# Kernel tuning notes

Hardware: AMD Instinct MI355X
Metric: run time of the kernel (lower is better)

Reference implementation:

```python
import jax, jax.numpy as jnp
import numpy as np
import math

B, D_MODEL, H, D_K, L = 24, 128, 8, 16, 512


def setup_inputs() -> dict:
    key = jax.random.key(0)
    ks = jax.random.split(key, 5)
    x = jax.random.normal(ks[0], (B, D_MODEL, L), dtype=jnp.float32)
    Wq = jax.random.normal(ks[1], (H, B, D_K, D_MODEL), dtype=jnp.float32)
    Wk = jax.random.normal(ks[2], (H, B, D_K, D_MODEL), dtype=jnp.float32)
    Wv = jax.random.normal(ks[3], (H, B, D_K, D_MODEL), dtype=jnp.float32)
    Wo = jax.random.normal(ks[4], (B, H * D_K, D_MODEL), dtype=jnp.float32)
    return {"x": x, "Wq": Wq, "Wk": Wk, "Wv": Wv, "Wo": Wo}


def reference(x, Wq, Wk, Wv, Wo):
    # Per-head, per-batch projections: [h,b,k,d] @ [b,d,l] -> [h,b,k,l]
    Q = jnp.einsum('hbkd,bdl->hbkl', Wq, x)
    K = jnp.einsum('hbkd,bdl->hbkl', Wk, x)
    V = jnp.einsum('hbkd,bdl->hbkl', Wv, x)
    # scores[h,b,l,m] = Q[:, :, :, l] . K[:, :, :, m]; torch softmax dim=1 of
    # the [B, L, L] score -> softmax over the QUERY axis l (axis=2 here).
    scores = jnp.einsum('hbkl,hbkm->hblm', Q, K) / math.sqrt(D_K)
    attn = jax.nn.softmax(scores, axis=2)
    # head_i = V @ attn : [h,b,v,l] @ [h,b,l,m] -> [h,b,v,m]
    heads = jnp.einsum('hbvl,hblm->hbvm', V, attn)
    # concat heads along channel dim: [b, h*v, L]
    head = heads.transpose(1, 0, 2, 3).reshape(B, H * D_K, L)
    # out = Wo @ head : [b, h*v, d_model] treated as [b,128,128] @ [b,128,L]
    out = jnp.einsum('bod,bdl->bol', Wo, head)
    return out
```

## Files before the change

kernel.cpp:

```cpp
#include <hip/hip_runtime.h>
#include <math.h>

#define NB 24
#define DM 128
#define NH 8
#define DK 16
#define LL 512
#define HB (NH * NB)

#define XTH_OFF 0
#define XTL_OFF 3145728
#define HT_OFF  6291456

typedef __attribute__((ext_vector_type(8))) short bf16x8;
typedef __attribute__((ext_vector_type(4))) float f32x4;
typedef __attribute__((ext_vector_type(4))) int   i32x4;

#define MFMA  __builtin_amdgcn_mfma_f32_16x16x32_bf16
#define EXP2  __builtin_amdgcn_exp2f
#define BPERM __builtin_amdgcn_ds_bpermute

static __device__ __forceinline__ unsigned bfr(float x) {
    return (__float_as_uint(x) + 0x8000u) & 0xffff0000u;
}

static __device__ __forceinline__ unsigned cvtpk(float a, float b) {
    unsigned r;
    asm("v_cvt_pk_bf16_f32 %0, %1, %2" : "=v"(r) : "v"(a), "v"(b));
    return r;
}

static __device__ __forceinline__ void wsplit(const float* __restrict__ p,
                                              bf16x8& aH, bf16x8& aL) {
    const float4 f0 = *(const float4*)p;
    const float4 f1 = *(const float4*)(p + 4);
    const float f[8] = {f0.x, f0.y, f0.z, f0.w, f1.x, f1.y, f1.z, f1.w};
    i32x4 h, l;
    #pragma unroll
    for (int q = 0; q < 4; ++q) {
        const unsigned h0 = bfr(f[2 * q]), h1 = bfr(f[2 * q + 1]);
        const unsigned e0 = bfr(f[2 * q]     - __uint_as_float(h0));
        const unsigned e1 = bfr(f[2 * q + 1] - __uint_as_float(h1));
        h[q] = (int)((h0 >> 16) | (h1 & 0xffff0000u));
        l[q] = (int)((e0 >> 16) | (e1 & 0xffff0000u));
    }
    aH = __builtin_bit_cast(bf16x8, h);
    aL = __builtin_bit_cast(bf16x8, l);
}

__global__ __launch_bounds__(256)
void prep(const float* __restrict__ x,
          unsigned short* __restrict__ xthi,
          unsigned short* __restrict__ xtlo)
{
    __shared__ float T[64][65];
    const int bid = blockIdx.x, tid = threadIdx.x;
    const int b = bid >> 3, lc = bid & 7;

    #pragma unroll
    for (int half = 0; half < 2; ++half) {
        const int d0 = half << 6;
        const float* __restrict__ xb =
            x + (size_t)b * 65536 + (size_t)d0 * LL + lc * 64;
        if (half) __syncthreads();
        #pragma unroll
        for (int i = 0; i < 16; ++i) {
            const int idx = i * 256 + tid;
            T[idx >> 6][idx & 63] = xb[(size_t)(idx >> 6) * LL + (idx & 63)];
        }
        __syncthreads();
        #pragma unroll
        for (int i = 0; i < 8; ++i) {
            const int idx = (i * 256 + tid) * 2;
            const int l = idx >> 6, dd = idx & 63;
            const float v0 = T[dd][l], v1 = T[dd + 1][l];
            const unsigned h0 = bfr(v0), h1 = bfr(v1);
            const unsigned e0 = bfr(v0 - __uint_as_float(h0));
            const unsigned e1 = bfr(v1 - __uint_as_float(h1));
            const size_t o = (size_t)b * 65536 +
                             (size_t)(lc * 64 + l) * DM + d0 + dd;
            *(unsigned*)(xthi + o) = (h0 >> 16) | (h1 & 0xffff0000u);
            *(unsigned*)(xtlo + o) = (e0 >> 16) | (e1 & 0xffff0000u);
        }
    }
}

static __device__ __forceinline__ void soft_pv(
    const f32x4& s0, const f32x4& s1, float tm, float& bar, float& sm,
    f32x4& O, const bf16x8& aV, int aLo, int aHi, bool up)
{
    const float nb = fmaxf(bar, tm + 32.f);
    const float f  = EXP2(bar - nb);
    bar = nb;
    const float e0 = EXP2(s0[0] - nb), e1 = EXP2(s0[1] - nb);
    const float e2 = EXP2(s0[2] - nb), e3 = EXP2(s0[3] - nb);
    const float e4 = EXP2(s1[0] - nb), e5 = EXP2(s1[1] - nb);
    const float e6 = EXP2(s1[2] - nb), e7 = EXP2(s1[3] - nb);
    const float sacc = ((e0 + e1) + (e2 + e3)) + ((e4 + e5) + (e6 + e7));
    sm = fmaf(sm, f, sacc);
    O *= f;
    const unsigned c0 = cvtpk(e0, e1), c1 = cvtpk(e2, e3);
    const unsigned c2 = cvtpk(e4, e5), c3 = cvtpk(e6, e7);
    const int p00 = BPERM(aLo, (int)c0), p02 = BPERM(aLo, (int)c2);
    const int p10 = BPERM(aLo, (int)c1), p12 = BPERM(aLo, (int)c3);
    const int p20 = BPERM(aHi, (int)c0), p22 = BPERM(aHi, (int)c2);
    const int p30 = BPERM(aHi, (int)c1), p32 = BPERM(aHi, (int)c3);
    i32x4 bi = { up ? p00 : p02, up ? p10 : p12,
                 up ? p20 : p22, up ? p30 : p32 };
    O = MFMA(aV, __builtin_bit_cast(bf16x8, bi), O, 0, 0, 0);
}

#define QK_STRIDE 40
#define V_STRIDE  520
#define KROWS     256

__global__ __launch_bounds__(512, 4)
void qkv_attn(const unsigned short* __restrict__ xthi,
              const unsigned short* __restrict__ xtlo,
              const float* __restrict__ Wq,
              const float* __restrict__ Wk,
              const float* __restrict__ Wv,
              unsigned short* __restrict__ ht)
{
    __shared__ unsigned short qs[LL * QK_STRIDE];
    __shared__ unsigned short ks[KROWS * QK_STRIDE];
    __shared__ unsigned short vs[DK * V_STRIDE];

    const int hb    = blockIdx.x >> 1;
    const int mhalf = blockIdx.x & 1;
    const int b     = hb % NB;
    const int wv    = threadIdx.x >> 6;
    const int lane  = threadIdx.x & 63;
    const int g     = lane >> 4;
    const int mR    = lane & 15;
    const int lQ    = wv * 64;
    const int kloc  = wv * 32;

    {
        const float* __restrict__ wqp = Wq + (size_t)hb * 2048 + mR * 128 + g * 8;
        const float* __restrict__ wkp = Wk + (size_t)hb * 2048 + mR * 128 + g * 8;
        const float* __restrict__ wvp = Wv + (size_t)hb * 2048 + mR * 128 + g * 8;
        const unsigned short* __restrict__ xh = xthi + (size_t)b * 65536 + g * 8;
        const unsigned short* __restrict__ xl = xtlo + (size_t)b * 65536 + g * 8;

        f32x4 CQ[4], CV[4], CK[2];
        #pragma unroll
        for (int t = 0; t < 4; ++t) {
            CQ[t] = (f32x4){0.f, 0.f, 0.f, 0.f};
            CV[t] = (f32x4){0.f, 0.f, 0.f, 0.f};
        }
        CK[0] = (f32x4){0.f, 0.f, 0.f, 0.f};
        CK[1] = (f32x4){0.f, 0.f, 0.f, 0.f};

        #pragma unroll
        for (int kk = 0; kk < 4; ++kk) {
            bf16x8 aH, aL;
            {
                bf16x8 kH[2], kL[2];
                #pragma unroll
                for (int t = 0; t < 2; ++t) {
                    const size_t ro =
                        (size_t)(mhalf * 256 + kloc + t * 16 + mR) * DM + kk * 32;
                    kH[t] = *(const bf16x8*)(xh + ro);
                    kL[t] = *(const bf16x8*)(xl + ro);
                }
                wsplit(wkp + kk * 32, aH, aL);
                #pragma unroll
                for (int t = 0; t < 2; ++t) {
                    CK[t] = MFMA(aH, kH[t], CK[t], 0, 0, 0);
                    CK[t] = MFMA(aH, kL[t], CK[t], 0, 0, 0);
                    CK[t] = MFMA(aL, kH[t], CK[t], 0, 0, 0);
                }
            }
            bf16x8 bH[4], bL[4];
            #pragma unroll
            for (int t = 0; t < 4; ++t) {
                const size_t ro = (size_t)(lQ + t * 16 + mR) * DM + kk * 32;
                bH[t] = *(const bf16x8*)(xh + ro);
                bL[t] = *(const bf16x8*)(xl + ro);
            }
            wsplit(wqp + kk * 32, aH, aL);
            #pragma unroll
            for (int t = 0; t < 4; ++t) {
                CQ[t] = MFMA(aH, bH[t], CQ[t], 0, 0, 0);
                CQ[t] = MFMA(aH, bL[t], CQ[t], 0, 0, 0);
                CQ[t] = MFMA(aL, bH[t], CQ[t], 0, 0, 0);
            }
            wsplit(wvp + kk * 32, aH, aL);
            #pragma unroll
            for (int t = 0; t < 4; ++t) {
                CV[t] = MFMA(aH, bH[t], CV[t], 0, 0, 0);
                CV[t] = MFMA(aH, bL[t], CV[t], 0, 0, 0);
                CV[t] = MFMA(aL, bH[t], CV[t], 0, 0, 0);
            }
        }

        #pragma unroll
        for (int t = 0; t < 4; ++t) {
            const int l = lQ + t * 16 + mR;
            #pragma unroll
            for (int i = 0; i < 4; ++i)
                vs[(4 * g + i) * V_STRIDE + l] =
                    (unsigned short)(bfr(CV[t][i]) >> 16);
        }
        #pragma unroll
        for (int t = 0; t < 4; ++t) {
            const int l = lQ + t * 16 + mR;
            ushort4 hi4, lo4;
            #pragma unroll
            for (int i = 0; i < 4; ++i) {
                const float v = CQ[t][i];
                const unsigned h = bfr(v);
                const unsigned lw = bfr(v - __uint_as_float(h));
                ((unsigned short*)&hi4)[i] = (unsigned short)(h >> 16);
                ((unsigned short*)&lo4)[i] = (unsigned short)(lw >> 16);
            }
            *(ushort4*)(qs + l * QK_STRIDE + 4 * g)      = hi4;
            *(ushort4*)(qs + l * QK_STRIDE + 16 + 4 * g) = lo4;
        }
        #pragma unroll
        for (int t = 0; t < 2; ++t) {
            const int r = kloc + t * 16 + mR;
            ushort4 hi4, lo4;
            #pragma unroll
            for (int i = 0; i < 4; ++i) {
                const float v = CK[t][i] * (0.25f * 1.44269504f);
                const unsigned h = bfr(v);
                const unsigned lw = bfr(v - __uint_as_float(h));
                ((unsigned short*)&hi4)[i] = (unsigned short)(h >> 16);
                ((unsigned short*)&lo4)[i] = (unsigned short)(lw >> 16);
            }
            *(ushort4*)(ks + r * QK_STRIDE + 4 * g)      = hi4;
            *(ushort4*)(ks + r * QK_STRIDE + 16 + 4 * g) = lo4;
        }
    }

    __syncthreads();

    const unsigned short* Kr0 = ks + (kloc + mR) * QK_STRIDE;
    const unsigned short* Kr1 = Kr0 + 16 * QK_STRIDE;
    const bf16x8 K0  = *(const bf16x8*)(Kr0 + g * 8);
    const bf16x8 K0s = *(const bf16x8*)(Kr0 + (g ^ 2) * 8);
    const bf16x8 K1  = *(const bf16x8*)(Kr1 + g * 8);
    const bf16x8 K1s = *(const bf16x8*)(Kr1 + (g ^ 2) * 8);

    const unsigned short* qrow = qs + mR * QK_STRIDE + g * 8;
    const unsigned short* vrow = vs + mR * V_STRIDE + g * 8;

    f32x4 O0 = {0.f,0.f,0.f,0.f}, O1 = {0.f,0.f,0.f,0.f};
    float bar0 = -1e30f, bar1 = -1e30f, sm0 = 0.f, sm1 = 0.f;

    const int aLo = ((g & 1) * 32 + mR) * 4;
    const int aHi = aLo + 64;
    const bool up = (g < 2);

    for (int l = 0; l < LL; l += 32) {
        const bf16x8 aQ0 = *(const bf16x8*)(qrow + l * QK_STRIDE);
        const bf16x8 aQ1 = *(const bf16x8*)(qrow + (l + 16) * QK_STRIDE);
        const bf16x8 aV  = *(const bf16x8*)(vrow + l);

        const f32x4 z = {0.f,0.f,0.f,0.f};
        f32x4 sA0 = MFMA(aQ0, K0, z, 0,0,0);   sA0 = MFMA(aQ0, K0s, sA0, 0,0,0);
        f32x4 sB0 = MFMA(aQ0, K1, z, 0,0,0);   sB0 = MFMA(aQ0, K1s, sB0, 0,0,0);
        f32x4 sA1 = MFMA(aQ1, K0, z, 0,0,0);   sA1 = MFMA(aQ1, K0s, sA1, 0,0,0);
        f32x4 sB1 = MFMA(aQ1, K1, z, 0,0,0);   sB1 = MFMA(aQ1, K1s, sB1, 0,0,0);

        float tmA = fmaxf(fmaxf(fmaxf(sA0[0],sA0[1]), fmaxf(sA0[2],sA0[3])),
                          fmaxf(fmaxf(sA1[0],sA1[1]), fmaxf(sA1[2],sA1[3])));
        float tmB = fmaxf(fmaxf(fmaxf(sB0[0],sB0[1]), fmaxf(sB0[2],sB0[3])),
                          fmaxf(fmaxf(sB1[0],sB1[1]), fmaxf(sB1[2],sB1[3])));
        tmA = fmaxf(tmA, __shfl_xor(tmA, 16, 64));
        tmA = fmaxf(tmA, __shfl_xor(tmA, 32, 64));
        tmB = fmaxf(tmB, __shfl_xor(tmB, 16, 64));
        tmB = fmaxf(tmB, __shfl_xor(tmB, 32, 64));

        const bool pA = __any(tmA + 64.f > bar0);
        const bool pB = __any(tmB + 64.f > bar1);
        if (pA) soft_pv(sA0, sA1, tmA, bar0, sm0, O0, aV, aLo, aHi, up);
        if (pB) soft_pv(sB0, sB1, tmB, bar1, sm1, O1, aV, aLo, aHi, up);
    }

    sm0 += __shfl_xor(sm0, 16, 64);  sm0 += __shfl_xor(sm0, 32, 64);
    sm1 += __shfl_xor(sm1, 16, 64);  sm1 += __shfl_xor(sm1, 32, 64);
    const float i0 = 1.f / sm0, i1 = 1.f / sm1;

    const int h = hb / NB, bb = hb % NB;
    const int mb = mhalf * 256 + kloc;
    unsigned short* __restrict__ ho =
        ht + (size_t)bb * 65536 + (size_t)(mb + mR) * DM + h * 16 + 4 * g;
    ushort4 p0, p1;
    #pragma unroll
    for (int i = 0; i < 4; ++i) {
        ((unsigned short*)&p0)[i] = (unsigned short)(bfr(O0[i] * i0) >> 16);
        ((unsigned short*)&p1)[i] = (unsigned short)(bfr(O1[i] * i1) >> 16);
    }
    *(ushort4*)ho             = p0;
    *(ushort4*)(ho + 16 * DM) = p1;
}

__global__ __launch_bounds__(256)
void out_mfma(const float* __restrict__ Wo,
              const unsigned short* __restrict__ ht,
              float* __restrict__ out)
{
    const int blk  = blockIdx.x;
    const int b    = blk >> 5;
    const int mq   = (blk >> 4) & 1;
    const int nq   = blk & 15;
    const int wv   = threadIdx.x >> 6;
    const int lane = threadIdx.x & 63;
    const int g = lane >> 4, mR = lane & 15;
    const int m0 = (mq * 4 + wv) * 16;
    const int n0 = nq * 32;

    const float* __restrict__ A =
        Wo + (size_t)b * 16384 + (size_t)(m0 + mR) * DM + g * 8;
    const unsigned short* __restrict__ B = ht + (size_t)b * 65536 + g * 8;

    f32x4 C0 = {0.f,0.f,0.f,0.f}, C1 = {0.f,0.f,0.f,0.f};
    #pragma unroll
    for (int kk = 0; kk < 4; ++kk) {
        const float4 f0 = *(const float4*)(A + kk * 32);
        const float4 f1 = *(const float4*)(A + kk * 32 + 4);
        i32x4 w;
        w[0] = (int)cvtpk(f0.x, f0.y);
        w[1] = (int)cvtpk(f0.z, f0.w);
        w[2] = (int)cvtpk(f1.x, f1.y);
        w[3] = (int)cvtpk(f1.z, f1.w);
        const bf16x8 aW = __builtin_bit_cast(bf16x8, w);
        const bf16x8 b0 = *(const bf16x8*)(B + (size_t)(n0 + mR) * DM + kk * 32);
        const bf16x8 b1 = *(const bf16x8*)(B + (size_t)(n0 + 16 + mR) * DM + kk * 32);
        C0 = MFMA(aW, b0, C0, 0, 0, 0);
        C1 = MFMA(aW, b1, C1, 0, 0, 0);
    }

    float* __restrict__ ob = out + (size_t)b * 65536 + (size_t)(m0 + 4 * g) * LL;
    #pragma unroll
    for (int i = 0; i < 4; ++i) {
        ob[(size_t)i * LL + n0 + mR]      = C0[i];
        ob[(size_t)i * LL + n0 + 16 + mR] = C1[i];
    }
}

extern "C" void kernel_launch(void* const* d_in, const int* in_sizes, int n_in,
                              void* d_out, int out_size, void* d_ws, size_t ws_size,
                              hipStream_t stream) {
    const float* x  = (const float*)d_in[0];
    const float* Wq = (const float*)d_in[1];
    const float* Wk = (const float*)d_in[2];
    const float* Wv = (const float*)d_in[3];
    const float* Wo = (const float*)d_in[4];
    float* out = (float*)d_out;

    char* ws = (char*)d_ws;
    unsigned short* xthi = (unsigned short*)(ws + XTH_OFF);
    unsigned short* xtlo = (unsigned short*)(ws + XTL_OFF);
    unsigned short* ht   = (unsigned short*)(ws + HT_OFF);

    prep     <<<192,     256, 0, stream>>>(x, xthi, xtlo);
    qkv_attn <<<HB * 2,  512, 0, stream>>>(xthi, xtlo, Wq, Wk, Wv, ht);
    out_mfma <<<NB * 32, 256, 0, stream>>>(Wo, ht, out);
}
```

Baseline: 129.9 us.

## Merge query-half blocks into one 1024-thread block per head-batch

Each (head,batch) pair is now handled by a single 1024-thread block instead of two 512-thread blocks that split the key axis. Every wave computes Q, K and V for its own 32 positions, so the duplicated Q/V projection over the full sequence in both half-blocks is removed. K shared memory grows to the full sequence length. The cost is fewer blocks (192 instead of 384) with larger LDS footprint and larger block size, which can lower occupancy and leave CUs underused on a 256-CU device.

```diff
diff --git a/kernel.cpp b/kernel.cpp
--- a/kernel.cpp
+++ b/kernel.cpp
@@ -112,9 +112,8 @@
 
 #define QK_STRIDE 40
 #define V_STRIDE  520
-#define KROWS     256
-
-__global__ __launch_bounds__(512, 4)
+
+__global__ __launch_bounds__(1024)
 void qkv_attn(const unsigned short* __restrict__ xthi,
               const unsigned short* __restrict__ xtlo,
               const float* __restrict__ Wq,
@@ -123,18 +122,16 @@
               unsigned short* __restrict__ ht)
 {
     __shared__ unsigned short qs[LL * QK_STRIDE];
-    __shared__ unsigned short ks[KROWS * QK_STRIDE];
+    __shared__ unsigned short ks[LL * QK_STRIDE];
     __shared__ unsigned short vs[DK * V_STRIDE];
 
-    const int hb    = blockIdx.x >> 1;
-    const int mhalf = blockIdx.x & 1;
+    const int hb    = blockIdx.x;
     const int b     = hb % NB;
     const int wv    = threadIdx.x >> 6;
     const int lane  = threadIdx.x & 63;
     const int g     = lane >> 4;
     const int mR    = lane & 15;
-    const int lQ    = wv * 64;
-    const int kloc  = wv * 32;
+    const int lQ    = wv * 32;
 
     {
         const float* __restrict__ wqp = Wq + (size_t)hb * 2048 + mR * 128 + g * 8;
@@ -143,52 +140,41 @@
         const unsigned short* __restrict__ xh = xthi + (size_t)b * 65536 + g * 8;
         const unsigned short* __restrict__ xl = xtlo + (size_t)b * 65536 + g * 8;
 
-        f32x4 CQ[4], CV[4], CK[2];
-        #pragma unroll
-        for (int t = 0; t < 4; ++t) {
+        f32x4 CQ[2], CK[2], CV[2];
+        #pragma unroll
+        for (int t = 0; t < 2; ++t) {
             CQ[t] = (f32x4){0.f, 0.f, 0.f, 0.f};
+            CK[t] = (f32x4){0.f, 0.f, 0.f, 0.f};
             CV[t] = (f32x4){0.f, 0.f, 0.f, 0.f};
         }
-        CK[0] = (f32x4){0.f, 0.f, 0.f, 0.f};
-        CK[1] = (f32x4){0.f, 0.f, 0.f, 0.f};
 
         #pragma unroll
         for (int kk = 0; kk < 4; ++kk) {
-            bf16x8 aH, aL;
-            {
-                bf16x8 kH[2], kL[2];
-                #pragma unroll
-                for (int t = 0; t < 2; ++t) {
-                    const size_t ro =
-                        (size_t)(mhalf * 256 + kloc + t * 16 + mR) * DM + kk * 32;
-                    kH[t] = *(const bf16x8*)(xh + ro);
-                    kL[t] = *(const bf16x8*)(xl + ro);
-                }
-                wsplit(wkp + kk * 32, aH, aL);
-                #pragma unroll
-                for (int t = 0; t < 2; ++t) {
-                    CK[t] = MFMA(aH, kH[t], CK[t], 0, 0, 0);
-                    CK[t] = MFMA(aH, kL[t], CK[t], 0, 0, 0);
-                    CK[t] = MFMA(aL, kH[t], CK[t], 0, 0, 0);
-                }
-            }
-            bf16x8 bH[4], bL[4];
-            #pragma unroll
-            for (int t = 0; t < 4; ++t) {
+            bf16x8 bH[2], bL[2];
+            #pragma unroll
+            for (int t = 0; t < 2; ++t) {
                 const size_t ro = (size_t)(lQ + t * 16 + mR) * DM + kk * 32;
                 bH[t] = *(const bf16x8*)(xh + ro);
                 bL[t] = *(const bf16x8*)(xl + ro);
             }
+            bf16x8 aH, aL;
             wsplit(wqp + kk * 32, aH, aL);
             #pragma unroll
-            for (int t = 0; t < 4; ++t) {
+            for (int t = 0; t < 2; ++t) {
                 CQ[t] = MFMA(aH, bH[t], CQ[t], 0, 0, 0);
                 CQ[t] = MFMA(aH, bL[t], CQ[t], 0, 0, 0);
                 CQ[t] = MFMA(aL, bH[t], CQ[t], 0, 0, 0);
             }
+            wsplit(wkp + kk * 32, aH, aL);
+            #pragma unroll
+            for (int t = 0; t < 2; ++t) {
+                CK[t] = MFMA(aH, bH[t], CK[t], 0, 0, 0);
+                CK[t] = MFMA(aH, bL[t], CK[t], 0, 0, 0);
+                CK[t] = MFMA(aL, bH[t], CK[t], 0, 0, 0);
+            }
             wsplit(wvp + kk * 32, aH, aL);
             #pragma unroll
-            for (int t = 0; t < 4; ++t) {
+            for (int t = 0; t < 2; ++t) {
                 CV[t] = MFMA(aH, bH[t], CV[t], 0, 0, 0);
                 CV[t] = MFMA(aH, bL[t], CV[t], 0, 0, 0);
                 CV[t] = MFMA(aL, bH[t], CV[t], 0, 0, 0);
@@ -196,7 +182,7 @@
         }
 
         #pragma unroll
-        for (int t = 0; t < 4; ++t) {
+        for (int t = 0; t < 2; ++t) {
             const int l = lQ + t * 16 + mR;
             #pragma unroll
             for (int i = 0; i < 4; ++i)
@@ -204,7 +190,7 @@
                     (unsigned short)(bfr(CV[t][i]) >> 16);
         }
         #pragma unroll
-        for (int t = 0; t < 4; ++t) {
+        for (int t = 0; t < 2; ++t) {
             const int l = lQ + t * 16 + mR;
             ushort4 hi4, lo4;
             #pragma unroll
@@ -220,7 +206,7 @@
         }
         #pragma unroll
         for (int t = 0; t < 2; ++t) {
-            const int r = kloc + t * 16 + mR;
+            const int r = lQ + t * 16 + mR;
             ushort4 hi4, lo4;
             #pragma unroll
             for (int i = 0; i < 4; ++i) {
@@ -237,6 +223,7 @@
 
     __syncthreads();
 
+    const int kloc = wv * 32;
     const unsigned short* Kr0 = ks + (kloc + mR) * QK_STRIDE;
     const unsigned short* Kr1 = Kr0 + 16 * QK_STRIDE;
     const bf16x8 K0  = *(const bf16x8*)(Kr0 + g * 8);
@@ -285,9 +272,8 @@
     const float i0 = 1.f / sm0, i1 = 1.f / sm1;
 
     const int h = hb / NB, bb = hb % NB;
-    const int mb = mhalf * 256 + kloc;
     unsigned short* __restrict__ ho =
-        ht + (size_t)bb * 65536 + (size_t)(mb + mR) * DM + h * 16 + 4 * g;
+        ht + (size_t)bb * 65536 + (size_t)(kloc + mR) * DM + h * 16 + 4 * g;
     ushort4 p0, p1;
     #pragma unroll
     for (int i = 0; i < 4; ++i) {
@@ -357,7 +343,7 @@
     unsigned short* xtlo = (unsigned short*)(ws + XTL_OFF);
     unsigned short* ht   = (unsigned short*)(ws + HT_OFF);
 
-    prep     <<<192,     256, 0, stream>>>(x, xthi, xtlo);
-    qkv_attn <<<HB * 2,  512, 0, stream>>>(xthi, xtlo, Wq, Wk, Wv, ht);
-    out_mfma <<<NB * 32, 256, 0, stream>>>(Wo, ht, out);
-}
+    prep     <<<192,     256,  0, stream>>>(x, xthi, xtlo);
+    qkv_attn <<<HB,      1024, 0, stream>>>(xthi, xtlo, Wq, Wk, Wv, ht);
+    out_mfma <<<NB * 32, 256,  0, stream>>>(Wo, ht, out);
+}
```

Measured after the change: 117.0 us. 10.0% less time.
